# Optimization experiments

Measured on AMD Instinct MI355X. Metric: run time of the kernel, lower is better.

## Reference

```python
import jax
import jax.numpy as jnp
import numpy as np
from jax import lax

B, T, D = 32, 256, 512   # batch, seq len, controller_dim (== memory_dim)
S = 2048                 # memory_slots
EPS_LN = 1e-5            # nn.LayerNorm default eps
EPS_NRM = 1e-12          # F.normalize default eps


def setup_inputs() -> dict:
    key = jax.random.key(0)
    ks = jax.random.split(key, 12)
    sc = 1.0 / np.sqrt(D)  # roughly torch Linear init scale
    return {
        "controller_seq": jax.random.normal(ks[0], (B, T, D), dtype=jnp.float32),
        "memory": jax.random.normal(ks[1], (S, D), dtype=jnp.float32),
        "Wk": jax.random.normal(ks[2], (D, D), dtype=jnp.float32) * sc,
        "bk": jax.random.normal(ks[3], (D,), dtype=jnp.float32) * sc,
        "We": jax.random.normal(ks[4], (D, D), dtype=jnp.float32) * sc,
        "be": jax.random.normal(ks[5], (D,), dtype=jnp.float32) * sc,
        "Ww": jax.random.normal(ks[6], (D, D), dtype=jnp.float32) * sc,
        "bw": jax.random.normal(ks[7], (D,), dtype=jnp.float32) * sc,
        "Wg": jax.random.normal(ks[8], (D, D), dtype=jnp.float32) * sc,
        "bg": jax.random.normal(ks[9], (D,), dtype=jnp.float32) * sc,
        "gamma": jnp.ones((D,), dtype=jnp.float32),
        "beta": jnp.zeros((D,), dtype=jnp.float32),
    }


def _l2norm(x, axis=-1):
    # matches F.normalize: x / max(||x||, eps)
    n = jnp.sqrt(jnp.sum(x * x, axis=axis, keepdims=True))
    return x / jnp.maximum(n, EPS_NRM)


def _layernorm(x, gamma, beta):
    mu = jnp.mean(x, axis=-1, keepdims=True)
    var = jnp.mean((x - mu) ** 2, axis=-1, keepdims=True)
    return (x - mu) * lax.rsqrt(var + EPS_LN) * gamma + beta


def reference(controller_seq, memory, Wk, bk, We, be, Ww, bw, Wg, bg, gamma, beta):
    batch = controller_seq.shape[0]

    def step(mem, c):  # mem: [S, Dm], c: [B, Dc]
        # --- read (addressing by cosine similarity) ---
        k = c @ Wk.T + bk                       # [B, Dm]
        sim = _l2norm(k) @ _l2norm(mem).T       # [B, S]
        w = jax.nn.softmax(sim, axis=-1)        # [B, S]
        read_val = w @ mem                      # [B, Dm]
        # --- write (erase / add, averaged over batch) ---
        erase = jax.nn.sigmoid(c @ We.T + be)   # [B, Dm]
        add = c @ Ww.T + bw                     # [B, Dm]
        # mean_b (1 - w_bs * e_bd) = 1 - (w^T e)/B ; avoids [B,S,Dm] intermediate
        erase_m = 1.0 - jnp.einsum("bs,bd->sd", w, erase) / batch
        add_m = jnp.einsum("bs,bd->sd", w, add) / batch
        new_mem = _layernorm(mem * erase_m + add_m, gamma, beta)  # dropout in eval mode
        # --- gated output ---
        g = jax.nn.sigmoid(c @ Wg.T + bg)       # [B, Dm]
        out_t = g * c + (1.0 - g) * read_val
        return new_mem, out_t

    _, outs = lax.scan(step, memory, jnp.swapaxes(controller_seq, 0, 1))  # outs: [T, B, D]
    return jnp.swapaxes(outs, 0, 1)  # [B, T, D]
```

## Files before the change

### kernel.cpp

```cpp
#include <hip/hip_runtime.h>

#define DEV __device__ __forceinline__

namespace {
constexpr int Bc = 32;
constexpr int Tc = 256;
constexpr int Dc = 512;
constexpr int Sc = 2048;
constexpr int NBLK = 256;
constexpr int NW   = 128;
constexpr int ROWS = Sc / NW;

constexpr size_t OFF_KN   = 0;
constexpr size_t OFF_E    = OFF_KN  + (size_t)Tc * Bc * Dc;
constexpr size_t OFF_A    = OFF_E   + (size_t)Tc * Bc * Dc;
constexpr size_t OFF_MEM  = OFF_A   + (size_t)Tc * Bc * Dc;
constexpr size_t OFF_EW   = OFF_MEM + (size_t)2 * Sc * Dc;
constexpr size_t OFF_RP   = OFF_EW  + (size_t)2 * Sc * Bc;
constexpr size_t OFF_DEN  = OFF_RP  + (size_t)2 * 16 * Bc * Dc;
constexpr size_t OFF_DENP = OFF_DEN + (size_t)Tc * Bc;
constexpr size_t OFF_FLAGS= OFF_DENP+ (size_t)2 * NW * Bc;
constexpr size_t OFF_GO   = OFF_FLAGS + 256 * 16;
}

DEV float sigm(float x) { return 1.0f / (1.0f + __expf(-x)); }

DEV float ld1cg(const float* p) {
  unsigned u = __hip_atomic_load((const unsigned*)p, __ATOMIC_RELAXED,
                                 __HIP_MEMORY_SCOPE_AGENT);
  return __uint_as_float(u);
}
DEV void st1cg(float* p, float v) {
  __hip_atomic_store((unsigned*)p, __float_as_uint(v), __ATOMIC_RELAXED,
                     __HIP_MEMORY_SCOPE_AGENT);
}
DEV float2 ld2cg(const float* p) {
  unsigned long long u = __hip_atomic_load((const unsigned long long*)p,
                                           __ATOMIC_RELAXED, __HIP_MEMORY_SCOPE_AGENT);
  union { unsigned long long u; float2 f; } c; c.u = u; return c.f;
}
DEV void st2cg(float* p, float2 v) {
  union { float2 f; unsigned long long u; } c; c.f = v;
  __hip_atomic_store((unsigned long long*)p, c.u, __ATOMIC_RELAXED,
                     __HIP_MEMORY_SCOPE_AGENT);
}

__global__ __launch_bounds__(256) void k_gemm(
    const float* __restrict__ A,
    const float* __restrict__ Wk, const float* __restrict__ bk,
    const float* __restrict__ We, const float* __restrict__ be,
    const float* __restrict__ Ww, const float* __restrict__ bw,
    const float* __restrict__ Wg, const float* __restrict__ bg,
    float* __restrict__ ws, float* __restrict__ gout)
{
  __shared__ float As[32][68];
  __shared__ float Bs[32][68];

  const int bid = blockIdx.x;
  const int mat = bid >> 10;
  const int rem = bid & 1023;
  const int rt = rem >> 3, jt = rem & 7;
  const int rbase = rt * 64, jbase = jt * 64;

  const float* Wm; const float* bm;
  if      (mat == 0) { Wm = Wk; bm = bk; }
  else if (mat == 1) { Wm = We; bm = be; }
  else if (mat == 2) { Wm = Ww; bm = bw; }
  else               { Wm = Wg; bm = bg; }

  const int tid = threadIdx.x;
  const int lr = tid >> 2;
  const int lk = (tid & 3) * 8;
  const int ty = tid >> 4, tx = tid & 15;

  float acc[4][4] = {};

  for (int k0 = 0; k0 < Dc; k0 += 32) {
    const float4 a0 = *(const float4*)&A [(size_t)(rbase + lr) * Dc + k0 + lk];
    const float4 a1 = *(const float4*)&A [(size_t)(rbase + lr) * Dc + k0 + lk + 4];
    const float4 b0 = *(const float4*)&Wm[(size_t)(jbase + lr) * Dc + k0 + lk];
    const float4 b1 = *(const float4*)&Wm[(size_t)(jbase + lr) * Dc + k0 + lk + 4];
    __syncthreads();
    As[lk + 0][lr] = a0.x; As[lk + 1][lr] = a0.y; As[lk + 2][lr] = a0.z; As[lk + 3][lr] = a0.w;
    As[lk + 4][lr] = a1.x; As[lk + 5][lr] = a1.y; As[lk + 6][lr] = a1.z; As[lk + 7][lr] = a1.w;
    Bs[lk + 0][lr] = b0.x; Bs[lk + 1][lr] = b0.y; Bs[lk + 2][lr] = b0.z; Bs[lk + 3][lr] = b0.w;
    Bs[lk + 4][lr] = b1.x; Bs[lk + 5][lr] = b1.y; Bs[lk + 6][lr] = b1.z; Bs[lk + 7][lr] = b1.w;
    __syncthreads();
    #pragma unroll
    for (int kk = 0; kk < 32; ++kk) {
      const float4 av = *(const float4*)&As[kk][ty * 4];
      const float4 bv = *(const float4*)&Bs[kk][tx * 4];
      const float ar[4] = {av.x, av.y, av.z, av.w};
      const float br[4] = {bv.x, bv.y, bv.z, bv.w};
      #pragma unroll
      for (int i = 0; i < 4; ++i)
        #pragma unroll
        for (int j = 0; j < 4; ++j)
          acc[i][j] = fmaf(ar[i], br[j], acc[i][j]);
    }
  }

  const float4 bias = *(const float4*)&bm[jbase + tx * 4];
  const float bi[4] = {bias.x, bias.y, bias.z, bias.w};
  #pragma unroll
  for (int i = 0; i < 4; ++i) {
    const int r = rbase + ty * 4 + i;
    float v[4];
    #pragma unroll
    for (int j = 0; j < 4; ++j) {
      v[j] = acc[i][j] + bi[j];
      if (mat & 1) v[j] = sigm(v[j]);
    }
    float4 o; o.x = v[0]; o.y = v[1]; o.z = v[2]; o.w = v[3];
    if (mat == 3) {
      *(float4*)&gout[(size_t)r * Dc + jbase + tx * 4] = o;
    } else {
      float* dst = ws + (mat == 0 ? OFF_KN : (mat == 1 ? OFF_E : OFF_A));
      const int t = r & 255, b = r >> 8;
      *(float4*)&dst[((size_t)t * Bc + b) * Dc + jbase + tx * 4] = o;
    }
  }
}

__global__ __launch_bounds__(256) void k_knorm(float* __restrict__ kn)
{
  const int row = blockIdx.x * 4 + (threadIdx.x >> 6);
  const int lane = threadIdx.x & 63;
  float* p = kn + (size_t)row * Dc;
  float4 v0 = *(const float4*)&p[lane * 4];
  float4 v1 = *(const float4*)&p[256 + lane * 4];
  float ss = v0.x*v0.x + v0.y*v0.y + v0.z*v0.z + v0.w*v0.w
           + v1.x*v1.x + v1.y*v1.y + v1.z*v1.z + v1.w*v1.w;
  #pragma unroll
  for (int off = 32; off >= 1; off >>= 1) ss += __shfl_xor(ss, off);
  const float inv = 1.0f / fmaxf(sqrtf(ss), 1e-12f);
  v0.x *= inv; v0.y *= inv; v0.z *= inv; v0.w *= inv;
  v1.x *= inv; v1.y *= inv; v1.z *= inv; v1.w *= inv;
  *(float4*)&p[lane * 4] = v0;
  *(float4*)&p[256 + lane * 4] = v1;
}

DEV void gbar(unsigned* flags, unsigned* go, unsigned step, int bid, int tid,
              int do_agg, const float* denp_par, float* den_out, float* lds_red)
{
  __syncthreads();
  if (bid == 0) {
    if (tid > 0) {
      while (__hip_atomic_load(&flags[tid * 16], __ATOMIC_RELAXED,
                               __HIP_MEMORY_SCOPE_AGENT) < step)
        __builtin_amdgcn_s_sleep(2);
    }
    __syncthreads();
    if (do_agg) {
      const int b = tid & 31, ch = tid >> 5;
      float s = 0.f;
      #pragma unroll
      for (int g = 0; g < 16; ++g)
        s += ld1cg(&denp_par[(size_t)(ch * 16 + g) * Bc + b]);
      lds_red[tid] = s;
      __syncthreads();
      if (tid < 32) {
        float tot = 0.f;
        #pragma unroll
        for (int c2 = 0; c2 < 8; ++c2) tot += lds_red[c2 * 32 + tid];
        st1cg(&den_out[tid], tot);
      }
    }
    __syncthreads();
    if (tid == 0)
      __hip_atomic_store(go, step, __ATOMIC_RELAXED, __HIP_MEMORY_SCOPE_AGENT);
  } else {
    if (tid == 0) {
      __hip_atomic_store(&flags[bid * 16], step, __ATOMIC_RELAXED,
                         __HIP_MEMORY_SCOPE_AGENT);
      while (__hip_atomic_load(go, __ATOMIC_RELAXED,
                               __HIP_MEMORY_SCOPE_AGENT) < step)
        __builtin_amdgcn_s_sleep(2);
    }
    __syncthreads();
  }
}

DEV void sim_phase(const float* __restrict__ knp, float* __restrict__ ewn,
                   float* __restrict__ denp_row, const float (*y)[516],
                   float* __restrict__ ew_own,
                   const float* invn_s, float* sred, int s0, int tid)
{
  const int r = tid >> 4, bp = tid & 15;
  const float* k0p = knp + (size_t)bp * Dc;
  const float* k1p = knp + (size_t)(bp + 16) * Dc;
  float acc0 = 0.f, acc1 = 0.f;
  #pragma unroll 4
  for (int dq = 0; dq < Dc / 4; ++dq) {
    const float4 y4 = *(const float4*)&y[r][dq * 4];
    const float4 ka = *(const float4*)&k0p[dq * 4];
    const float4 kb = *(const float4*)&k1p[dq * 4];
    acc0 = fmaf(y4.x, ka.x, acc0); acc0 = fmaf(y4.y, ka.y, acc0);
    acc0 = fmaf(y4.z, ka.z, acc0); acc0 = fmaf(y4.w, ka.w, acc0);
    acc1 = fmaf(y4.x, kb.x, acc1); acc1 = fmaf(y4.y, kb.y, acc1);
    acc1 = fmaf(y4.z, kb.z, acc1); acc1 = fmaf(y4.w, kb.w, acc1);
  }
  const float iv = invn_s[r];
  const float e0 = __expf(acc0 * iv);
  const float e1 = __expf(acc1 * iv);
  st1cg(&ewn[(size_t)(s0 + r) * Bc + bp], e0);
  st1cg(&ewn[(size_t)(s0 + r) * Bc + bp + 16], e1);
  ew_own[r * 32 + bp]      = e0;
  ew_own[r * 32 + bp + 16] = e1;
  if (tid < 32) sred[tid] = 0.f;
  __syncthreads();
  atomicAdd(&sred[bp], e0);
  atomicAdd(&sred[bp + 16], e1);
  __syncthreads();
  if (tid < 32) st1cg(&denp_row[tid], sred[tid]);
}

__global__ __launch_bounds__(256) void k_main(
    const float* __restrict__ cs, const float* __restrict__ mem_in,
    const float* __restrict__ gamma, const float* __restrict__ beta,
    float* __restrict__ ws, float* __restrict__ out)
{
  __shared__ float mrows[16][516];
  __shared__ float xbuf[16][516];
  __shared__ float ew_own[16 * 32];
  __shared__ float wbuf[16][32];
  __shared__ float lds_red[256];
  __shared__ float sred[32];
  __shared__ float mu_s[16], rs_s[16], invn_s[16], dinv_s[32];

  float* kn   = ws + OFF_KN;
  float* eptb = ws + OFF_E;
  float* aptb = ws + OFF_A;
  float* memb = ws + OFF_MEM;
  float* ewb  = ws + OFF_EW;
  float* rp   = ws + OFF_RP;
  float* den  = ws + OFF_DEN;
  float* denp = ws + OFF_DENP;
  unsigned* flags = (unsigned*)(ws + OFF_FLAGS);
  unsigned* go    = (unsigned*)(ws + OFF_GO);

  const int bid = blockIdx.x, tid = threadIdx.x;
  const float inv32 = 1.0f / 32.0f;

  if (bid < NW) {
    const int s0 = bid * ROWS;
    const int c0 = tid * 2;
    #pragma unroll
    for (int r = 0; r < ROWS; ++r) {
      const float2 m = *(const float2*)&mem_in[(size_t)(s0 + r) * Dc + c0];
      *(float2*)&mrows[r][c0] = m;
      st2cg(&memb[(size_t)(s0 + r) * Dc + c0], m);
    }
    __syncthreads();
    {
      const int row = tid >> 4, li = tid & 15;
      float ss = 0.f;
      #pragma unroll
      for (int i = 0; i < 8; ++i) {
        const float4 v = *(const float4*)&mrows[row][(li + i * 16) * 4];
        ss += v.x*v.x + v.y*v.y + v.z*v.z + v.w*v.w;
      }
      ss += __shfl_xor(ss, 8); ss += __shfl_xor(ss, 4);
      ss += __shfl_xor(ss, 2); ss += __shfl_xor(ss, 1);
      if (li == 0) invn_s[row] = 1.0f / fmaxf(sqrtf(ss), 1e-12f);
    }
    __syncthreads();
    sim_phase(kn, ewb, denp + (size_t)bid * Bc, mrows, ew_own,
              invn_s, sred, s0, tid);
  }
  gbar(flags, go, 1u, bid, tid, 1, denp, den, lds_red);

  for (int t = 0; t <= Tc; ++t) {
    if (bid < NW) {
      if (t < Tc - 1) {
        const int s0 = bid * ROWS;
        const int c0 = tid * 2;
        float* ewn  = ewb  + (size_t)((t + 1) & 1) * Sc * Bc;
        float* memn = memb + (size_t)((t + 1) & 1) * Sc * Dc;
        float* denp_n = denp + (size_t)((t + 1) & 1) * NW * Bc + (size_t)bid * Bc;

        if (tid < 32) dinv_s[tid] = 1.0f / ld1cg(&den[(size_t)t * Bc + tid]);
        __syncthreads();
        for (int idx = tid; idx < ROWS * 32; idx += 256)
          wbuf[idx >> 5][idx & 31] = ew_own[idx] * dinv_s[idx & 31];
        __syncthreads();

        float2 er[ROWS] = {}, ad[ROWS] = {};
        const float* ept = eptb + (size_t)t * Bc * Dc;
        const float* apt = aptb + (size_t)t * Bc * Dc;
        #pragma unroll 4
        for (int b = 0; b < 32; ++b) {
          const float2 ev = *(const float2*)&ept[(size_t)b * Dc + c0];
          const float2 av = *(const float2*)&apt[(size_t)b * Dc + c0];
          #pragma unroll
          for (int r = 0; r < ROWS; ++r) {
            const float wv = wbuf[r][b];
            er[r].x = fmaf(wv, ev.x, er[r].x); er[r].y = fmaf(wv, ev.y, er[r].y);
            ad[r].x = fmaf(wv, av.x, ad[r].x); ad[r].y = fmaf(wv, av.y, ad[r].y);
          }
        }
        float2 xr[ROWS];
        #pragma unroll
        for (int r = 0; r < ROWS; ++r) {
          const float2 m = *(const float2*)&mrows[r][c0];
          float2 x;
          x.x = m.x * (1.0f - er[r].x * inv32) + ad[r].x * inv32;
          x.y = m.y * (1.0f - er[r].y * inv32) + ad[r].y * inv32;
          xr[r] = x;
          *(float2*)&xbuf[r][c0] = x;
        }
        __syncthreads();
        {
          const int row = tid >> 4, li = tid & 15;
          float s1 = 0.f, s2 = 0.f;
          #pragma unroll
          for (int i = 0; i < 8; ++i) {
            const float4 v = *(const float4*)&xbuf[row][(li + i * 16) * 4];
            s1 += v.x + v.y + v.z + v.w;
            s2 += v.x*v.x + v.y*v.y + v.z*v.z + v.w*v.w;
          }
          s1 += __shfl_xor(s1, 8); s2 += __shfl_xor(s2, 8);
          s1 += __shfl_xor(s1, 4); s2 += __shfl_xor(s2, 4);
          s1 += __shfl_xor(s1, 2); s2 += __shfl_xor(s2, 2);
          s1 += __shfl_xor(s1, 1); s2 += __shfl_xor(s2, 1);
          if (li == 0) {
            const float mu = s1 * (1.0f / 512.0f);
            const float var = s2 * (1.0f / 512.0f) - mu * mu;
            mu_s[row] = mu;
            rs_s[row] = rsqrtf(var + 1e-5f);
          }
        }
        __syncthreads();
        const float2 gm  = *(const float2*)&gamma[c0];
        const float2 bt2 = *(const float2*)&beta[c0];
        #pragma unroll
        for (int r = 0; r < ROWS; ++r) {
          const float mu = mu_s[r], rs = rs_s[r];
          float2 y;
          y.x = (xr[r].x - mu) * rs * gm.x + bt2.x;
          y.y = (xr[r].y - mu) * rs * gm.y + bt2.y;
          *(float2*)&mrows[r][c0] = y;
          st2cg(&memn[(size_t)(s0 + r) * Dc + c0], y);
        }
        __syncthreads();
        {
          const int row = tid >> 4, li = tid & 15;
          float ss = 0.f;
          #pragma unroll
          for (int i = 0; i < 8; ++i) {
            const float4 v = *(const float4*)&mrows[row][(li + i * 16) * 4];
            ss += v.x*v.x + v.y*v.y + v.z*v.z + v.w*v.w;
          }
          ss += __shfl_xor(ss, 8); ss += __shfl_xor(ss, 4);
          ss += __shfl_xor(ss, 2); ss += __shfl_xor(ss, 1);
          if (li == 0) invn_s[row] = 1.0f / fmaxf(sqrtf(ss), 1e-12f);
        }
        __syncthreads();
        sim_phase(kn + (size_t)(t + 1) * Bc * Dc, ewn, denp_n, mrows, ew_own,
                  invn_s, sred, s0, tid);
      }
    } else {
      const int rb = bid - NW;
      if (rb < 8 && t >= 1) {
        const int t0 = t - 1;
        const float* rpc = rp + (size_t)(t0 & 1) * 16 * Bc * Dc;
        const int base = (rb * 256 + tid) * 8;
        const int b = base >> 9, d0 = base & 511;
        const float inv = 1.0f / ld1cg(&den[(size_t)t0 * Bc + b]);
        float r0[8] = {};
        #pragma unroll
        for (int si = 0; si < 16; ++si) {
          const float* q = rpc + ((size_t)si * Bc + b) * Dc + d0;
          const float2 p0 = ld2cg(q + 0);
          const float2 p1 = ld2cg(q + 2);
          const float2 p2 = ld2cg(q + 4);
          const float2 p3 = ld2cg(q + 6);
          r0[0] += p0.x; r0[1] += p0.y; r0[2] += p1.x; r0[3] += p1.y;
          r0[4] += p2.x; r0[5] += p2.y; r0[6] += p3.x; r0[7] += p3.y;
        }
        const size_t oofs = ((size_t)b * Tc + t0) * Dc + d0;
        const float4 g0 = *(const float4*)&out[oofs];
        const float4 g1 = *(const float4*)&out[oofs + 4];
        const float4 c0v = *(const float4*)&cs[oofs];
        const float4 c1v = *(const float4*)&cs[oofs + 4];
        float4 o0, o1;
        o0.x = g0.x * c0v.x + (1.0f - g0.x) * (r0[0] * inv);
        o0.y = g0.y * c0v.y + (1.0f - g0.y) * (r0[1] * inv);
        o0.z = g0.z * c0v.z + (1.0f - g0.z) * (r0[2] * inv);
        o0.w = g0.w * c0v.w + (1.0f - g0.w) * (r0[3] * inv);
        o1.x = g1.x * c1v.x + (1.0f - g1.x) * (r0[4] * inv);
        o1.y = g1.y * c1v.y + (1.0f - g1.y) * (r0[5] * inv);
        o1.z = g1.z * c1v.z + (1.0f - g1.z) * (r0[6] * inv);
        o1.w = g1.w * c1v.w + (1.0f - g1.w) * (r0[7] * inv);
        *(float4*)&out[oofs] = o0;
        *(float4*)&out[oofs + 4] = o1;
      }
      if (t < Tc) {
        const int si = rb >> 3, dj = rb & 7;
        const int sB = si * 128;
        const float* ewc = ewb + (size_t)(t & 1) * Sc * Bc;
        const float* memc = memb + (size_t)(t & 1) * Sc * Dc;
        float* ewl = (float*)xbuf;
        for (int i = tid; i < 128 * 32; i += 256)
          ewl[i] = ld1cg(&ewc[(size_t)sB * Bc + i]);
        __syncthreads();
        const int b = tid >> 3, dg = tid & 7;
        const int cbase = dj * 64 + dg * 8;
        float a0[8] = {};
        #pragma unroll 4
        for (int s = 0; s < 128; ++s) {
          const float wv = ewl[s * 32 + b];
          const float* mrow = memc + (size_t)(sB + s) * Dc + cbase;
          const float2 m0 = ld2cg(mrow + 0);
          const float2 m1 = ld2cg(mrow + 2);
          const float2 m2 = ld2cg(mrow + 4);
          const float2 m3 = ld2cg(mrow + 6);
          a0[0] = fmaf(wv, m0.x, a0[0]); a0[1] = fmaf(wv, m0.y, a0[1]);
          a0[2] = fmaf(wv, m1.x, a0[2]); a0[3] = fmaf(wv, m1.y, a0[3]);
          a0[4] = fmaf(wv, m2.x, a0[4]); a0[5] = fmaf(wv, m2.y, a0[5]);
          a0[6] = fmaf(wv, m3.x, a0[6]); a0[7] = fmaf(wv, m3.y, a0[7]);
        }
        float* dst = rp + (size_t)(t & 1) * 16 * Bc * Dc + ((size_t)si * Bc + b) * Dc + cbase;
        float2 w0; w0.x = a0[0]; w0.y = a0[1]; st2cg(dst + 0, w0);
        float2 w1; w1.x = a0[2]; w1.y = a0[3]; st2cg(dst + 2, w1);
        float2 w2; w2.x = a0[4]; w2.y = a0[5]; st2cg(dst + 4, w2);
        float2 w3; w3.x = a0[6]; w3.y = a0[7]; st2cg(dst + 6, w3);
      }
    }
    if (t < Tc) {
      const int do_agg = (t + 1 < Tc) ? 1 : 0;
      gbar(flags, go, (unsigned)(t + 2), bid, tid, do_agg,
           denp + (size_t)((t + 1) & 1) * NW * Bc,
           den + (size_t)(t + 1) * Bc, lds_red);
    }
  }
}

extern "C" void kernel_launch(void* const* d_in, const int* in_sizes, int n_in,
                              void* d_out, int out_size, void* d_ws, size_t ws_size,
                              hipStream_t stream)
{
  const float* cs    = (const float*)d_in[0];
  const float* mem   = (const float*)d_in[1];
  const float* Wk    = (const float*)d_in[2];
  const float* bk    = (const float*)d_in[3];
  const float* We    = (const float*)d_in[4];
  const float* be    = (const float*)d_in[5];
  const float* Ww    = (const float*)d_in[6];
  const float* bw    = (const float*)d_in[7];
  const float* Wg    = (const float*)d_in[8];
  const float* bg    = (const float*)d_in[9];
  const float* gamma = (const float*)d_in[10];
  const float* beta  = (const float*)d_in[11];
  float* ws  = (float*)d_ws;
  float* out = (float*)d_out;

  hipMemsetAsync(ws + OFF_FLAGS, 0, (256 * 16 + 1) * sizeof(unsigned), stream);

  hipLaunchKernelGGL(k_gemm, dim3(4096), dim3(256), 0, stream,
                     cs, Wk, bk, We, be, Ww, bw, Wg, bg, ws, out);
  hipLaunchKernelGGL(k_knorm, dim3(2048), dim3(256), 0, stream, ws + OFF_KN);
  hipLaunchKernelGGL(k_main, dim3(NBLK), dim3(256), 0, stream,
                     cs, mem, gamma, beta, ws, out);
}
```

Baseline: 12.12 ms.

## Compute read partials from on-chip memory rows and drop global memory copy

```diff
diff --git a/kernel.cpp b/kernel.cpp
--- a/kernel.cpp
+++ b/kernel.cpp
@@ -6,20 +6,16 @@
 constexpr int Bc = 32;
 constexpr int Tc = 256;
 constexpr int Dc = 512;
-constexpr int Sc = 2048;
 constexpr int NBLK = 256;
 constexpr int NW   = 128;
-constexpr int ROWS = Sc / NW;
+constexpr int ROWS = 16;
 
 constexpr size_t OFF_KN   = 0;
-constexpr size_t OFF_E    = OFF_KN  + (size_t)Tc * Bc * Dc;
-constexpr size_t OFF_A    = OFF_E   + (size_t)Tc * Bc * Dc;
-constexpr size_t OFF_MEM  = OFF_A   + (size_t)Tc * Bc * Dc;
-constexpr size_t OFF_EW   = OFF_MEM + (size_t)2 * Sc * Dc;
-constexpr size_t OFF_RP   = OFF_EW  + (size_t)2 * Sc * Bc;
-constexpr size_t OFF_DEN  = OFF_RP  + (size_t)2 * 16 * Bc * Dc;
-constexpr size_t OFF_DENP = OFF_DEN + (size_t)Tc * Bc;
-constexpr size_t OFF_FLAGS= OFF_DENP+ (size_t)2 * NW * Bc;
+constexpr size_t OFF_E    = OFF_KN + (size_t)Tc * Bc * Dc;
+constexpr size_t OFF_A    = OFF_E  + (size_t)Tc * Bc * Dc;
+constexpr size_t OFF_RP   = OFF_A  + (size_t)Tc * Bc * Dc;
+constexpr size_t OFF_DENP = OFF_RP + (size_t)2 * NW * Bc * Dc;
+constexpr size_t OFF_FLAGS= OFF_DENP + (size_t)2 * NW * Bc;
 constexpr size_t OFF_GO   = OFF_FLAGS + 256 * 16;
 }
 
@@ -140,8 +136,7 @@
   *(float4*)&p[256 + lane * 4] = v1;
 }
 
-DEV void gbar(unsigned* flags, unsigned* go, unsigned step, int bid, int tid,
-              int do_agg, const float* denp_par, float* den_out, float* lds_red)
+DEV void gbar(unsigned* flags, unsigned* go, unsigned step, int bid, int tid)
 {
   __syncthreads();
   if (bid == 0) {
@@ -149,22 +144,6 @@
       while (__hip_atomic_load(&flags[tid * 16], __ATOMIC_RELAXED,
                                __HIP_MEMORY_SCOPE_AGENT) < step)
         __builtin_amdgcn_s_sleep(2);
-    }
-    __syncthreads();
-    if (do_agg) {
-      const int b = tid & 31, ch = tid >> 5;
-      float s = 0.f;
-      #pragma unroll
-      for (int g = 0; g < 16; ++g)
-        s += ld1cg(&denp_par[(size_t)(ch * 16 + g) * Bc + b]);
-      lds_red[tid] = s;
-      __syncthreads();
-      if (tid < 32) {
-        float tot = 0.f;
-        #pragma unroll
-        for (int c2 = 0; c2 < 8; ++c2) tot += lds_red[c2 * 32 + tid];
-        st1cg(&den_out[tid], tot);
-      }
     }
     __syncthreads();
     if (tid == 0)
@@ -181,10 +160,9 @@
   }
 }
 
-DEV void sim_phase(const float* __restrict__ knp, float* __restrict__ ewn,
-                   float* __restrict__ denp_row, const float (*y)[516],
-                   float* __restrict__ ew_own,
-                   const float* invn_s, float* sred, int s0, int tid)
+DEV void sim_phase(const float* __restrict__ knp, float* __restrict__ denp_row,
+                   const float (*y)[516], float* __restrict__ ew_own,
+                   const float* invn_s, float* sred, int tid)
 {
   const int r = tid >> 4, bp = tid & 15;
   const float* k0p = knp + (size_t)bp * Dc;
@@ -203,8 +181,6 @@
   const float iv = invn_s[r];
   const float e0 = __expf(acc0 * iv);
   const float e1 = __expf(acc1 * iv);
-  st1cg(&ewn[(size_t)(s0 + r) * Bc + bp], e0);
-  st1cg(&ewn[(size_t)(s0 + r) * Bc + bp + 16], e1);
   ew_own[r * 32 + bp]      = e0;
   ew_own[r * 32 + bp + 16] = e1;
   if (tid < 32) sred[tid] = 0.f;
@@ -221,20 +197,17 @@
     float* __restrict__ ws, float* __restrict__ out)
 {
   __shared__ float mrows[16][516];
-  __shared__ float xbuf[16][516];
   __shared__ float ew_own[16 * 32];
   __shared__ float wbuf[16][32];
   __shared__ float lds_red[256];
+  __shared__ float2 red2[256];
   __shared__ float sred[32];
   __shared__ float mu_s[16], rs_s[16], invn_s[16], dinv_s[32];
 
   float* kn   = ws + OFF_KN;
   float* eptb = ws + OFF_E;
   float* aptb = ws + OFF_A;
-  float* memb = ws + OFF_MEM;
-  float* ewb  = ws + OFF_EW;
   float* rp   = ws + OFF_RP;
-  float* den  = ws + OFF_DEN;
   float* denp = ws + OFF_DENP;
   unsigned* flags = (unsigned*)(ws + OFF_FLAGS);
   unsigned* go    = (unsigned*)(ws + OFF_GO);
@@ -246,11 +219,8 @@
     const int s0 = bid * ROWS;
     const int c0 = tid * 2;
     #pragma unroll
-    for (int r = 0; r < ROWS; ++r) {
-      const float2 m = *(const float2*)&mem_in[(size_t)(s0 + r) * Dc + c0];
-      *(float2*)&mrows[r][c0] = m;
-      st2cg(&memb[(size_t)(s0 + r) * Dc + c0], m);
-    }
+    for (int r = 0; r < ROWS; ++r)
+      *(float2*)&mrows[r][c0] = *(const float2*)&mem_in[(size_t)(s0 + r) * Dc + c0];
     __syncthreads();
     {
       const int row = tid >> 4, li = tid & 15;
@@ -265,174 +235,169 @@
       if (li == 0) invn_s[row] = 1.0f / fmaxf(sqrtf(ss), 1e-12f);
     }
     __syncthreads();
-    sim_phase(kn, ewb, denp + (size_t)bid * Bc, mrows, ew_own,
-              invn_s, sred, s0, tid);
-  }
-  gbar(flags, go, 1u, bid, tid, 1, denp, den, lds_red);
+    sim_phase(kn, denp + (size_t)bid * Bc, mrows, ew_own, invn_s, sred, tid);
+  }
+  gbar(flags, go, 1u, bid, tid);
 
   for (int t = 0; t <= Tc; ++t) {
     if (bid < NW) {
-      if (t < Tc - 1) {
-        const int s0 = bid * ROWS;
+      if (t < Tc) {
         const int c0 = tid * 2;
-        float* ewn  = ewb  + (size_t)((t + 1) & 1) * Sc * Bc;
-        float* memn = memb + (size_t)((t + 1) & 1) * Sc * Dc;
-        float* denp_n = denp + (size_t)((t + 1) & 1) * NW * Bc + (size_t)bid * Bc;
-
-        if (tid < 32) dinv_s[tid] = 1.0f / ld1cg(&den[(size_t)t * Bc + tid]);
-        __syncthreads();
+        {
+          const float* dp = denp + (size_t)(t & 1) * NW * Bc;
+          const int b = tid & 31, ch = tid >> 5;
+          float s = 0.f;
+          #pragma unroll
+          for (int g = 0; g < 16; ++g)
+            s += ld1cg(&dp[(size_t)(ch * 16 + g) * Bc + b]);
+          lds_red[tid] = s;
+          __syncthreads();
+          if (tid < 32) {
+            float tot = 0.f;
+            #pragma unroll
+            for (int c2 = 0; c2 < 8; ++c2) tot += lds_red[c2 * 32 + tid];
+            dinv_s[tid] = 1.0f / tot;
+          }
+          __syncthreads();
+        }
         for (int idx = tid; idx < ROWS * 32; idx += 256)
           wbuf[idx >> 5][idx & 31] = ew_own[idx] * dinv_s[idx & 31];
         __syncthreads();
 
-        float2 er[ROWS] = {}, ad[ROWS] = {};
-        const float* ept = eptb + (size_t)t * Bc * Dc;
-        const float* apt = aptb + (size_t)t * Bc * Dc;
-        #pragma unroll 4
-        for (int b = 0; b < 32; ++b) {
-          const float2 ev = *(const float2*)&ept[(size_t)b * Dc + c0];
-          const float2 av = *(const float2*)&apt[(size_t)b * Dc + c0];
+        float2 mr[ROWS];
+        #pragma unroll
+        for (int r = 0; r < ROWS; ++r) mr[r] = *(const float2*)&mrows[r][c0];
+
+        {
+          float* rpd = rp + (size_t)(t & 1) * NW * Bc * Dc
+                          + (size_t)bid * Bc * Dc + c0;
+          #pragma unroll 4
+          for (int b = 0; b < 32; ++b) {
+            float2 a; a.x = 0.f; a.y = 0.f;
+            #pragma unroll
+            for (int r = 0; r < ROWS; ++r) {
+              const float wv = wbuf[r][b];
+              a.x = fmaf(wv, mr[r].x, a.x);
+              a.y = fmaf(wv, mr[r].y, a.y);
+            }
+            st2cg(rpd + (size_t)b * Dc, a);
+          }
+        }
+
+        if (t < Tc - 1) {
+          float2 er[ROWS] = {}, ad[ROWS] = {};
+          const float* ept = eptb + (size_t)t * Bc * Dc;
+          const float* apt = aptb + (size_t)t * Bc * Dc;
+          #pragma unroll 4
+          for (int b = 0; b < 32; ++b) {
+            const float2 ev = *(const float2*)&ept[(size_t)b * Dc + c0];
+            const float2 av = *(const float2*)&apt[(size_t)b * Dc + c0];
+            #pragma unroll
+            for (int r = 0; r < ROWS; ++r) {
+              const float wv = wbuf[r][b];
+              er[r].x = fmaf(wv, ev.x, er[r].x); er[r].y = fmaf(wv, ev.y, er[r].y);
+              ad[r].x = fmaf(wv, av.x, ad[r].x); ad[r].y = fmaf(wv, av.y, ad[r].y);
+            }
+          }
+          float2 xr[ROWS];
           #pragma unroll
           for (int r = 0; r < ROWS; ++r) {
-            const float wv = wbuf[r][b];
-            er[r].x = fmaf(wv, ev.x, er[r].x); er[r].y = fmaf(wv, ev.y, er[r].y);
-            ad[r].x = fmaf(wv, av.x, ad[r].x); ad[r].y = fmaf(wv, av.y, ad[r].y);
-          }
+            float2 x;
+            x.x = mr[r].x * (1.0f - er[r].x * inv32) + ad[r].x * inv32;
+            x.y = mr[r].y * (1.0f - er[r].y * inv32) + ad[r].y * inv32;
+            xr[r] = x;
+            *(float2*)&mrows[r][c0] = x;
+          }
+          __syncthreads();
+          {
+            const int row = tid >> 4, li = tid & 15;
+            float s1 = 0.f, s2 = 0.f;
+            #pragma unroll
+            for (int i = 0; i < 8; ++i) {
+              const float4 v = *(const float4*)&mrows[row][(li + i * 16) * 4];
+              s1 += v.x + v.y + v.z + v.w;
+              s2 += v.x*v.x + v.y*v.y + v.z*v.z + v.w*v.w;
+            }
+            s1 += __shfl_xor(s1, 8); s2 += __shfl_xor(s2, 8);
+            s1 += __shfl_xor(s1, 4); s2 += __shfl_xor(s2, 4);
+            s1 += __shfl_xor(s1, 2); s2 += __shfl_xor(s2, 2);
+            s1 += __shfl_xor(s1, 1); s2 += __shfl_xor(s2, 1);
+            if (li == 0) {
+              const float mu = s1 * (1.0f / 512.0f);
+              const float var = s2 * (1.0f / 512.0f) - mu * mu;
+              mu_s[row] = mu;
+              rs_s[row] = rsqrtf(var + 1e-5f);
+            }
+          }
+          __syncthreads();
+          const float2 gm  = *(const float2*)&gamma[c0];
+          const float2 bt2 = *(const float2*)&beta[c0];
+          #pragma unroll
+          for (int r = 0; r < ROWS; ++r) {
+            const float mu = mu_s[r], rs = rs_s[r];
+            float2 y;
+            y.x = (xr[r].x - mu) * rs * gm.x + bt2.x;
+            y.y = (xr[r].y - mu) * rs * gm.y + bt2.y;
+            *(float2*)&mrows[r][c0] = y;
+          }
+          __syncthreads();
+          {
+            const int row = tid >> 4, li = tid & 15;
+            float ss = 0.f;
+            #pragma unroll
+            for (int i = 0; i < 8; ++i) {
+              const float4 v = *(const float4*)&mrows[row][(li + i * 16) * 4];
+              ss += v.x*v.x + v.y*v.y + v.z*v.z + v.w*v.w;
+            }
+            ss += __shfl_xor(ss, 8); ss += __shfl_xor(ss, 4);
+            ss += __shfl_xor(ss, 2); ss += __shfl_xor(ss, 1);
+            if (li == 0) invn_s[row] = 1.0f / fmaxf(sqrtf(ss), 1e-12f);
+          }
+          __syncthreads();
+          sim_phase(kn + (size_t)(t + 1) * Bc * Dc,
+                    denp + (size_t)((t + 1) & 1) * NW * Bc + (size_t)bid * Bc,
+                    mrows, ew_own, invn_s, sred, tid);
         }
-        float2 xr[ROWS];
-        #pragma unroll
-        for (int r = 0; r < ROWS; ++r) {
-          const float2 m = *(const float2*)&mrows[r][c0];
-          float2 x;
-          x.x = m.x * (1.0f - er[r].x * inv32) + ad[r].x * inv32;
-          x.y = m.y * (1.0f - er[r].y * inv32) + ad[r].y * inv32;
-          xr[r] = x;
-          *(float2*)&xbuf[r][c0] = x;
+      }
+    } else {
+      if (t >= 1) {
+        const int t0 = t - 1;
+        const int rb = bid - NW;
+        const int b = rb >> 2;
+        const int d0 = (rb & 3) * 128;
+        const float* rpc = rp + (size_t)(t0 & 1) * NW * Bc * Dc
+                              + (size_t)b * Dc + d0;
+        const int jp = (tid & 63) * 2;
+        const int q  = tid >> 6;
+        float2 a; a.x = 0.f; a.y = 0.f;
+        #pragma unroll 4
+        for (int pi = 0; pi < 32; ++pi) {
+          const int p = q * 32 + pi;
+          const float2 v = ld2cg(rpc + (size_t)p * Bc * Dc + jp);
+          a.x += v.x; a.y += v.y;
+        }
+        red2[tid] = a;
+        __syncthreads();
+        if (tid < 64) {
+          const float2 v0 = red2[tid];
+          const float2 v1 = red2[64 + tid];
+          const float2 v2 = red2[128 + tid];
+          const float2 v3 = red2[192 + tid];
+          float2 rv;
+          rv.x = (v0.x + v1.x) + (v2.x + v3.x);
+          rv.y = (v0.y + v1.y) + (v2.y + v3.y);
+          const size_t oofs = ((size_t)b * Tc + t0) * Dc + d0 + tid * 2;
+          const float2 g  = *(const float2*)&out[oofs];
+          const float2 cv = *(const float2*)&cs[oofs];
+          float2 o;
+          o.x = g.x * cv.x + (1.0f - g.x) * rv.x;
+          o.y = g.y * cv.y + (1.0f - g.y) * rv.y;
+          *(float2*)&out[oofs] = o;
         }
         __syncthreads();
-        {
-          const int row = tid >> 4, li = tid & 15;
-          float s1 = 0.f, s2 = 0.f;
-          #pragma unroll
-          for (int i = 0; i < 8; ++i) {
-            const float4 v = *(const float4*)&xbuf[row][(li + i * 16) * 4];
-            s1 += v.x + v.y + v.z + v.w;
-            s2 += v.x*v.x + v.y*v.y + v.z*v.z + v.w*v.w;
-          }
-          s1 += __shfl_xor(s1, 8); s2 += __shfl_xor(s2, 8);
-          s1 += __shfl_xor(s1, 4); s2 += __shfl_xor(s2, 4);
-          s1 += __shfl_xor(s1, 2); s2 += __shfl_xor(s2, 2);
-          s1 += __shfl_xor(s1, 1); s2 += __shfl_xor(s2, 1);
-          if (li == 0) {
-            const float mu = s1 * (1.0f / 512.0f);
-            const float var = s2 * (1.0f / 512.0f) - mu * mu;
-            mu_s[row] = mu;
-            rs_s[row] = rsqrtf(var + 1e-5f);
-          }
-        }
-        __syncthreads();
-        const float2 gm  = *(const float2*)&gamma[c0];
-        const float2 bt2 = *(const float2*)&beta[c0];
-        #pragma unroll
-        for (int r = 0; r < ROWS; ++r) {
-          const float mu = mu_s[r], rs = rs_s[r];
-          float2 y;
-          y.x = (xr[r].x - mu) * rs * gm.x + bt2.x;
-          y.y = (xr[r].y - mu) * rs * gm.y + bt2.y;
-          *(float2*)&mrows[r][c0] = y;
-          st2cg(&memn[(size_t)(s0 + r) * Dc + c0], y);
-        }
-        __syncthreads();
-        {
-          const int row = tid >> 4, li = tid & 15;
-          float ss = 0.f;
-          #pragma unroll
-          for (int i = 0; i < 8; ++i) {
-            const float4 v = *(const float4*)&mrows[row][(li + i * 16) * 4];
-            ss += v.x*v.x + v.y*v.y + v.z*v.z + v.w*v.w;
-          }
-          ss += __shfl_xor(ss, 8); ss += __shfl_xor(ss, 4);
-          ss += __shfl_xor(ss, 2); ss += __shfl_xor(ss, 1);
-          if (li == 0) invn_s[row] = 1.0f / fmaxf(sqrtf(ss), 1e-12f);
-        }
-        __syncthreads();
-        sim_phase(kn + (size_t)(t + 1) * Bc * Dc, ewn, denp_n, mrows, ew_own,
-                  invn_s, sred, s0, tid);
       }
-    } else {
-      const int rb = bid - NW;
-      if (rb < 8 && t >= 1) {
-        const int t0 = t - 1;
-        const float* rpc = rp + (size_t)(t0 & 1) * 16 * Bc * Dc;
-        const int base = (rb * 256 + tid) * 8;
-        const int b = base >> 9, d0 = base & 511;
-        const float inv = 1.0f / ld1cg(&den[(size_t)t0 * Bc + b]);
-        float r0[8] = {};
-        #pragma unroll
-        for (int si = 0; si < 16; ++si) {
-          const float* q = rpc + ((size_t)si * Bc + b) * Dc + d0;
-          const float2 p0 = ld2cg(q + 0);
-          const float2 p1 = ld2cg(q + 2);
-          const float2 p2 = ld2cg(q + 4);
-          const float2 p3 = ld2cg(q + 6);
-          r0[0] += p0.x; r0[1] += p0.y; r0[2] += p1.x; r0[3] += p1.y;
-          r0[4] += p2.x; r0[5] += p2.y; r0[6] += p3.x; r0[7] += p3.y;
-        }
-        const size_t oofs = ((size_t)b * Tc + t0) * Dc + d0;
-        const float4 g0 = *(const float4*)&out[oofs];
-        const float4 g1 = *(const float4*)&out[oofs + 4];
-        const float4 c0v = *(const float4*)&cs[oofs];
-        const float4 c1v = *(const float4*)&cs[oofs + 4];
-        float4 o0, o1;
-        o0.x = g0.x * c0v.x + (1.0f - g0.x) * (r0[0] * inv);
-        o0.y = g0.y * c0v.y + (1.0f - g0.y) * (r0[1] * inv);
-        o0.z = g0.z * c0v.z + (1.0f - g0.z) * (r0[2] * inv);
-        o0.w = g0.w * c0v.w + (1.0f - g0.w) * (r0[3] * inv);
-        o1.x = g1.x * c1v.x + (1.0f - g1.x) * (r0[4] * inv);
-        o1.y = g1.y * c1v.y + (1.0f - g1.y) * (r0[5] * inv);
-        o1.z = g1.z * c1v.z + (1.0f - g1.z) * (r0[6] * inv);
-        o1.w = g1.w * c1v.w + (1.0f - g1.w) * (r0[7] * inv);
-        *(float4*)&out[oofs] = o0;
-        *(float4*)&out[oofs + 4] = o1;
-      }
-      if (t < Tc) {
-        const int si = rb >> 3, dj = rb & 7;
-        const int sB = si * 128;
-        const float* ewc = ewb + (size_t)(t & 1) * Sc * Bc;
-        const float* memc = memb + (size_t)(t & 1) * Sc * Dc;
-        float* ewl = (float*)xbuf;
-        for (int i = tid; i < 128 * 32; i += 256)
-          ewl[i] = ld1cg(&ewc[(size_t)sB * Bc + i]);
-        __syncthreads();
-        const int b = tid >> 3, dg = tid & 7;
-        const int cbase = dj * 64 + dg * 8;
-        float a0[8] = {};
-        #pragma unroll 4
-        for (int s = 0; s < 128; ++s) {
-          const float wv = ewl[s * 32 + b];
-          const float* mrow = memc + (size_t)(sB + s) * Dc + cbase;
-          const float2 m0 = ld2cg(mrow + 0);
-          const float2 m1 = ld2cg(mrow + 2);
-          const float2 m2 = ld2cg(mrow + 4);
-          const float2 m3 = ld2cg(mrow + 6);
-          a0[0] = fmaf(wv, m0.x, a0[0]); a0[1] = fmaf(wv, m0.y, a0[1]);
-          a0[2] = fmaf(wv, m1.x, a0[2]); a0[3] = fmaf(wv, m1.y, a0[3]);
-          a0[4] = fmaf(wv, m2.x, a0[4]); a0[5] = fmaf(wv, m2.y, a0[5]);
-          a0[6] = fmaf(wv, m3.x, a0[6]); a0[7] = fmaf(wv, m3.y, a0[7]);
-        }
-        float* dst = rp + (size_t)(t & 1) * 16 * Bc * Dc + ((size_t)si * Bc + b) * Dc + cbase;
-        float2 w0; w0.x = a0[0]; w0.y = a0[1]; st2cg(dst + 0, w0);
-        float2 w1; w1.x = a0[2]; w1.y = a0[3]; st2cg(dst + 2, w1);
-        float2 w2; w2.x = a0[4]; w2.y = a0[5]; st2cg(dst + 4, w2);
-        float2 w3; w3.x = a0[6]; w3.y = a0[7]; st2cg(dst + 6, w3);
-      }
-    }
-    if (t < Tc) {
-      const int do_agg = (t + 1 < Tc) ? 1 : 0;
-      gbar(flags, go, (unsigned)(t + 2), bid, tid, do_agg,
-           denp + (size_t)((t + 1) & 1) * NW * Bc,
-           den + (size_t)(t + 1) * Bc, lds_red);
-    }
+    }
+    if (t < Tc) gbar(flags, go, (unsigned)(t + 2), bid, tid);
   }
 }
 
```

Result: faster. 10.66 ms (-12.0%).
